# Kernel optimization log

Measured on AMD Instinct MI355X. Metric: run time of the kernel, lower is better.

The kernel has to match this reference:

```python
import jax, jax.numpy as jnp
import numpy as np

B, N, C = 16, 4096, 64
M, K, R = 1024, 32, 0.2
EPS = 1e-5  # BatchNorm eps (eval mode: running_mean=0, running_var=1)


def setup_inputs() -> dict:
    key = jax.random.key(0)
    ks = jax.random.split(key, 8)
    s = 0.05
    return {
        "points": jax.random.normal(ks[0], (B, 3, N), dtype=jnp.float32),
        "features": jax.random.normal(ks[1], (B, C, N), dtype=jnp.float32),
        "w1": jax.random.normal(ks[2], (64, 3 + C), dtype=jnp.float32) * s,
        "b1": jnp.zeros((64,), jnp.float32),
        "g1": jnp.ones((64,), jnp.float32),
        "be1": jnp.zeros((64,), jnp.float32),
        "w2": jax.random.normal(ks[3], (64, 64), dtype=jnp.float32) * s,
        "b2": jnp.zeros((64,), jnp.float32),
        "g2": jnp.ones((64,), jnp.float32),
        "be2": jnp.zeros((64,), jnp.float32),
        "w3": jax.random.normal(ks[4], (128, 64), dtype=jnp.float32) * s,
        "b3": jnp.zeros((128,), jnp.float32),
        "g3": jnp.ones((128,), jnp.float32),
        "be3": jnp.zeros((128,), jnp.float32),
    }


def farthest_point_sampling(pts, m):
    """pts: [B,N,3] -> indices [B,m] (iterative FPS, first point = index 0)."""
    b, n, _ = pts.shape

    def step(carry, _):
        dist, last = carry  # dist [b,n], last [b]
        lastp = jnp.take_along_axis(pts, last[:, None, None], axis=1)  # [b,1,3]
        d = jnp.sum((pts - lastp) ** 2, axis=-1)  # [b,n]
        dist = jnp.minimum(dist, d)
        nxt = jnp.argmax(dist, axis=1).astype(jnp.int32)
        return (dist, nxt), last

    init = (jnp.full((b, n), 1e10, pts.dtype), jnp.zeros((b,), jnp.int32))
    _, idx = jax.lax.scan(step, init, None, length=m)
    return idx.T  # [b,m]


def ball_query(pts, centroids, k, radius):
    """pts [B,N,3], centroids [B,M,3] -> neighbor indices [B,M,K].
    Takes the first k points (by index) within radius; pads with the first hit,
    matching the PointNet++ CUDA ball_query semantics."""
    n = pts.shape[1]
    p2 = jnp.sum(pts ** 2, -1)  # [B,N]
    c2 = jnp.sum(centroids ** 2, -1)  # [B,M]
    d2 = c2[:, :, None] + p2[:, None, :] - 2.0 * jnp.einsum("bmd,bnd->bmn", centroids, pts)
    ar = jnp.arange(n, dtype=jnp.int32)
    key = jnp.where(d2 <= radius * radius, ar[None, None, :], n)  # [B,M,N]
    idx = jnp.sort(key, axis=-1)[..., :k]  # first k in-radius indices (or n)
    first = idx[..., :1]  # centroid itself is always a hit (d2=0)
    idx = jnp.where(idx < n, idx, first)
    return jnp.clip(idx, 0, n - 1)


def _mlp_block(x, w, bias, g, be):
    # 1x1 Conv2d + BatchNorm (eval: mean=0, var=1) + ReLU, x: [B,M,K,Cin]
    y = jnp.einsum("oc,bmkc->bmko", w, x) + bias
    y = y * (g / jnp.sqrt(1.0 + EPS)) + be
    return jax.nn.relu(y)


def reference(points, features, w1, b1, g1, be1, w2, b2, g2, be2, w3, b3, g3, be3):
    pts = jnp.transpose(points, (0, 2, 1))  # [B,N,3]
    feats = jnp.transpose(features, (0, 2, 1))  # [B,N,C]
    b = pts.shape[0]

    cidx = farthest_point_sampling(pts, M)  # [B,M]
    bidx = jnp.arange(b)[:, None]
    cent = pts[bidx, cidx]  # [B,M,3]

    nidx = ball_query(pts, cent, K, R)  # [B,M,K]
    bidx2 = jnp.arange(b)[:, None, None]
    gpts = pts[bidx2, nidx]  # [B,M,K,3]
    gfeat = feats[bidx2, nidx]  # [B,M,K,C]
    local = gpts - cent[:, :, None, :]  # local coords
    x = jnp.concatenate([local, gfeat], axis=-1)  # [B,M,K,3+C]

    x = _mlp_block(x, w1, b1, g1, be1)
    x = _mlp_block(x, w2, b2, g2, be2)
    x = _mlp_block(x, w3, b3, g3, be3)

    out = jnp.max(x, axis=2)  # max over K samples -> [B,M,Cout]
    centroids = jnp.transpose(cent, (0, 2, 1))  # [B,3,M]
    out = jnp.transpose(out, (0, 2, 1))  # [B,Cout,M]
    return centroids, out
```

## Files before the change

kernel.cpp:

```cpp
#include <hip/hip_runtime.h>
#include <math.h>

#define NPTS 4096
#define MC   1024
#define KNB  32

typedef __attribute__((ext_vector_type(8))) short bf16x8;
typedef __attribute__((ext_vector_type(4))) float f32x4;

__device__ __forceinline__ unsigned short f2bf(float f) {
  unsigned int u = __float_as_uint(f);
  u = u + 0x7fffu + ((u >> 16) & 1u);
  return (unsigned short)(u >> 16);
}

template <int CTRL>
__device__ __forceinline__ void dpp_step64(unsigned int& hi, unsigned int& lo) {
  unsigned int ohi = (unsigned int)__builtin_amdgcn_update_dpp((int)hi, (int)hi, CTRL, 0xF, 0xF, false);
  unsigned int olo = (unsigned int)__builtin_amdgcn_update_dpp((int)lo, (int)lo, CTRL, 0xF, 0xF, false);
  if (ohi > hi || (ohi == hi && olo > lo)) { hi = ohi; lo = olo; }
}

__global__ __launch_bounds__(256, 1) void fps_kernel(const float* __restrict__ points,
                                                     float* __restrict__ out_cent) {
  __shared__ float sx[NPTS], sy[NPTS], sz[NPTS];
  __shared__ __align__(16) unsigned long long skey[2][4];
  __shared__ float slog[3][MC];
  const int b = blockIdx.x, t = threadIdx.x;
  const int w = t >> 6, lane = t & 63;
  const float* pb = points + (size_t)b * 3 * NPTS;

  float fx[16], fy[16], fz[16], dist[16];
#pragma unroll
  for (int k = 0; k < 4; ++k) {
    float4 X = ((const float4*)pb)[k * 256 + t];
    float4 Y = ((const float4*)(pb + NPTS))[k * 256 + t];
    float4 Z = ((const float4*)(pb + 2 * NPTS))[k * 256 + t];
    ((float4*)sx)[k * 256 + t] = X;
    ((float4*)sy)[k * 256 + t] = Y;
    ((float4*)sz)[k * 256 + t] = Z;
    fx[k * 4 + 0] = X.x; fx[k * 4 + 1] = X.y; fx[k * 4 + 2] = X.z; fx[k * 4 + 3] = X.w;
    fy[k * 4 + 0] = Y.x; fy[k * 4 + 1] = Y.y; fy[k * 4 + 2] = Y.z; fy[k * 4 + 3] = Y.w;
    fz[k * 4 + 0] = Z.x; fz[k * 4 + 1] = Z.y; fz[k * 4 + 2] = Z.z; fz[k * 4 + 3] = Z.w;
  }
#pragma unroll
  for (int j = 0; j < 16; ++j) dist[j] = 1e10f;
  __syncthreads();

  float lx = sx[0], ly = sy[0], lz = sz[0];

  for (int i = 0; i < MC; ++i) {
    if (t == 0) { slog[0][i] = lx; slog[1][i] = ly; slog[2][i] = lz; }
    if (i == MC - 1) break;

    float bv = -1.0f; int bi = 0;
#pragma unroll
    for (int k = 0; k < 4; ++k)
#pragma unroll
      for (int c = 0; c < 4; ++c) {
        int j = k * 4 + c;
        float dx = __fsub_rn(fx[j], lx);
        float dy = __fsub_rn(fy[j], ly);
        float dz = __fsub_rn(fz[j], lz);
        float d  = __fadd_rn(__fadd_rn(__fmul_rn(dx, dx), __fmul_rn(dy, dy)), __fmul_rn(dz, dz));
        float dm = fminf(dist[j], d);
        dist[j] = dm;
        if (dm > bv) { bv = dm; bi = k * 1024 + t * 4 + c; }
      }

    unsigned int hi = __float_as_uint(bv), lo = ~(unsigned int)bi;
    dpp_step64<0x111>(hi, lo);
    dpp_step64<0x112>(hi, lo);
    dpp_step64<0x114>(hi, lo);
    dpp_step64<0x118>(hi, lo);
    dpp_step64<0x142>(hi, lo);
    dpp_step64<0x143>(hi, lo);

    const int nb = i & 1;
    if (lane == 63) skey[nb][w] = ((unsigned long long)hi << 32) | lo;
    __syncthreads();

    unsigned long long k0 = skey[nb][0], k1 = skey[nb][1];
    unsigned long long k2 = skey[nb][2], k3 = skey[nb][3];
    unsigned long long ka = (k0 > k1) ? k0 : k1;
    unsigned long long kb = (k2 > k3) ? k2 : k3;
    unsigned long long km = (ka > kb) ? ka : kb;
    const int sel = (int)(~(unsigned int)km);

    lx = sx[sel]; ly = sy[sel]; lz = sz[sel];
  }
  __syncthreads();
  float* oc = out_cent + (size_t)b * 3 * MC;
#pragma unroll
  for (int k = 0; k < 12; ++k) {
    int idx = t + k * 256;
    oc[idx] = ((const float*)slog)[idx];
  }
}

__global__ __launch_bounds__(256) void transpose_feats(const float* __restrict__ feats,
                                                       unsigned short* __restrict__ featsT) {
  __shared__ float tile[64][65];
  const int blk = blockIdx.x;
  const int b = blk >> 6;
  const int n0 = (blk & 63) * 64;
  const int t = threadIdx.x;
  const float* src = feats + (size_t)b * 64 * NPTS;
  {
    const int n = t & 63, cbase = t >> 6;
#pragma unroll
    for (int j = 0; j < 16; ++j) {
      int c = cbase + j * 4;
      tile[c][n] = src[(size_t)c * NPTS + n0 + n];
    }
  }
  __syncthreads();
  {
    const int c = t & 63, nbase = t >> 6;
    unsigned short* dst = featsT + ((size_t)b * NPTS + n0) * 64;
#pragma unroll
    for (int j = 0; j < 16; ++j) {
      int n = nbase + j * 4;
      dst[(size_t)n * 64 + c] = f2bf(tile[c][n]);
    }
  }
}

__global__ __launch_bounds__(64) void pack_w(const float* __restrict__ w1,
                                             const float* __restrict__ w2,
                                             const float* __restrict__ w3,
                                             unsigned short* __restrict__ wpack) {
  const int f = blockIdx.x, lane = threadIdx.x;
  int layer, kt, nt;
  if (f < 12)      { layer = 0; kt = f >> 2;        nt = f & 3; }
  else if (f < 20) { layer = 1; kt = (f - 12) >> 2; nt = (f - 12) & 3; }
  else             { layer = 2; kt = (f - 20) >> 3; nt = (f - 20) & 7; }
  const int o = nt * 16 + (lane & 15);
  unsigned short* dst = wpack + ((size_t)f * 64 + lane) * 8;
#pragma unroll
  for (int j = 0; j < 8; ++j) {
    int k = kt * 32 + (lane >> 4) * 8 + j;
    float x = 0.0f;
    if (layer == 0)      { if (k < 67) { int cin = (k < 64) ? (k + 3) : (k - 64); x = w1[o * 67 + cin]; } }
    else if (layer == 1) { x = w2[o * 64 + k]; }
    else                 { x = w3[o * 64 + k]; }
    dst[j] = f2bf(x);
  }
}

__global__ __launch_bounds__(256) void ball_query_kernel(const float* __restrict__ points,
                                                         const float* __restrict__ cent,
                                                         int* __restrict__ nidx) {
  __shared__ float sx[NPTS], sy[NPTS], sz[NPTS];
  __shared__ int lists[4][KNB];
  const int b  = blockIdx.x >> 4;
  const int cb = blockIdx.x & 15;
  const int t = threadIdx.x;
  const float* pb = points + (size_t)b * 3 * NPTS;
#pragma unroll
  for (int j = 0; j < 4; ++j) {
    int i4 = t + j * 256;
    ((float4*)sx)[i4] = ((const float4*)pb)[i4];
    ((float4*)sy)[i4] = ((const float4*)(pb + NPTS))[i4];
    ((float4*)sz)[i4] = ((const float4*)(pb + 2 * NPTS))[i4];
  }
  __syncthreads();
  const int w = t >> 6, lane = t & 63;
  const float R2 = (float)(0.2 * 0.2);
  const float* cbp = cent + (size_t)b * 3 * MC;
  for (int cm = 0; cm < 16; ++cm) {
    const int m  = cb * 64 + w * 16 + cm;
    const int bm = b * MC + m;
    const float cx = cbp[m], cy = cbp[MC + m], cz = cbp[2 * MC + m];
    const float c2 = __fadd_rn(__fadd_rn(__fmul_rn(cx, cx), __fmul_rn(cy, cy)), __fmul_rn(cz, cz));
    int cnt = 0;
    for (int ch = 0; ch < 64; ++ch) {
      const int n = ch * 64 + lane;
      float x = sx[n], y = sy[n], z = sz[n];
      float p2  = __fadd_rn(__fadd_rn(__fmul_rn(x, x),  __fmul_rn(y, y)),  __fmul_rn(z, z));
      float dot = __fadd_rn(__fadd_rn(__fmul_rn(cx, x), __fmul_rn(cy, y)), __fmul_rn(cz, z));
      float d2  = __fsub_rn(__fadd_rn(c2, p2), __fmul_rn(2.0f, dot));
      bool hit = (d2 <= R2);
      unsigned long long msk = __ballot(hit);
      if (hit) {
        int pos = cnt + __popcll(msk & ((1ull << lane) - 1ull));
        if (pos < KNB) lists[w][pos] = n;
      }
      cnt += __popcll(msk);
      if (cnt >= KNB) break;
    }
    if (lane < KNB) {
      int first = lists[w][0];
      int v = (lane < cnt) ? lists[w][lane] : first;
      nidx[(size_t)bm * KNB + lane] = v;
    }
  }
}

__global__ __launch_bounds__(256) void mlp_kernel(
    const float* __restrict__ points,
    const float* __restrict__ cent,
    const int* __restrict__ nidx,
    const unsigned short* __restrict__ featsT,
    const unsigned short* __restrict__ wpack,
    const float* __restrict__ b1, const float* __restrict__ g1, const float* __restrict__ be1,
    const float* __restrict__ b2, const float* __restrict__ g2, const float* __restrict__ be2,
    const float* __restrict__ b3, const float* __restrict__ g3, const float* __restrict__ be3,
    float* __restrict__ out) {
  __shared__ __align__(16) unsigned short Hs[4][2][32 * 72];
  __shared__ __align__(16) float obuf[128 * 20];
  const int t = threadIdx.x;
  const int w = t >> 6, lane = t & 63;
  const int r = lane & 15, q = lane >> 4;
  const float inv_s = 1.0f / sqrtf(1.0f + 1e-5f);

  float pb1[4], ps1[4], pe1[4], pb2[4], ps2[4], pe2[4], pb3[8], ps3[8], pe3[8];
#pragma unroll
  for (int nt = 0; nt < 4; ++nt) {
    int o = nt * 16 + r;
    pb1[nt] = b1[o]; ps1[nt] = g1[o] * inv_s; pe1[nt] = be1[o];
    pb2[nt] = b2[o]; ps2[nt] = g2[o] * inv_s; pe2[nt] = be2[o];
  }
#pragma unroll
  for (int nt = 0; nt < 8; ++nt) {
    int o = nt * 16 + r;
    pb3[nt] = b3[o]; ps3[nt] = g3[o] * inv_s; pe3[nt] = be3[o];
  }
  const int bm0 = blockIdx.x * 16;
  const int b   = bm0 >> 10;
  const int m0  = bm0 & 1023;
  const float* ptsb = points + (size_t)b * 3 * NPTS;
  const float* cbp  = cent + (size_t)b * 3 * MC;

  for (int it = 0; it < 4; ++it) {
    const int ml = it * 4 + w;
    const int bm = bm0 + ml;
    const int m  = bm & 1023;
    const int n0 = nidx[(size_t)bm * KNB + r];
    const int n1 = nidx[(size_t)bm * KNB + 16 + r];
    const float cx = cbp[m], cy = cbp[MC + m], cz = cbp[2 * MC + m];

    bf16x8 aF[2][2];
#pragma unroll
    for (int mt = 0; mt < 2; ++mt) {
      int n = mt ? n1 : n0;
      const unsigned short* rowp = featsT + ((size_t)b * NPTS + n) * 64 + q * 8;
      aF[mt][0] = *(const bf16x8*)(rowp);
      aF[mt][1] = *(const bf16x8*)(rowp + 32);
    }
    bf16x8 aL[2];
#pragma unroll
    for (int mt = 0; mt < 2; ++mt) {
      bf16x8 a = {0, 0, 0, 0, 0, 0, 0, 0};
      if (q == 0) {
        int n = mt ? n1 : n0;
        a[0] = (short)f2bf(ptsb[n] - cx);
        a[1] = (short)f2bf(ptsb[NPTS + n] - cy);
        a[2] = (short)f2bf(ptsb[2 * NPTS + n] - cz);
      }
      aL[mt] = a;
    }
    f32x4 acc1[2][4];
#pragma unroll
    for (int mt = 0; mt < 2; ++mt)
#pragma unroll
      for (int nt = 0; nt < 4; ++nt) acc1[mt][nt] = (f32x4){0.f, 0.f, 0.f, 0.f};
#pragma unroll
    for (int kt = 0; kt < 3; ++kt) {
#pragma unroll
      for (int nt = 0; nt < 4; ++nt) {
        bf16x8 wf = *(const bf16x8*)(wpack + ((size_t)(kt * 4 + nt) * 64 + lane) * 8);
#pragma unroll
        for (int mt = 0; mt < 2; ++mt) {
          bf16x8 a = (kt < 2) ? aF[mt][kt] : aL[mt];
          acc1[mt][nt] = __builtin_amdgcn_mfma_f32_16x16x32_bf16(a, wf, acc1[mt][nt], 0, 0, 0);
        }
      }
    }
#pragma unroll
    for (int mt = 0; mt < 2; ++mt)
#pragma unroll
      for (int nt = 0; nt < 4; ++nt)
#pragma unroll
        for (int rr = 0; rr < 4; ++rr) {
          float y = (acc1[mt][nt][rr] + pb1[nt]) * ps1[nt] + pe1[nt];
          y = fmaxf(y, 0.0f);
          Hs[w][0][(mt * 16 + q * 4 + rr) * 72 + nt * 16 + r] = f2bf(y);
        }
    __threadfence_block();

    f32x4 acc2[2][4];
#pragma unroll
    for (int mt = 0; mt < 2; ++mt)
#pragma unroll
      for (int nt = 0; nt < 4; ++nt) acc2[mt][nt] = (f32x4){0.f, 0.f, 0.f, 0.f};
#pragma unroll
    for (int kt = 0; kt < 2; ++kt) {
      bf16x8 a0 = *(const bf16x8*)&Hs[w][0][(0 * 16 + r) * 72 + kt * 32 + q * 8];
      bf16x8 a1 = *(const bf16x8*)&Hs[w][0][(1 * 16 + r) * 72 + kt * 32 + q * 8];
#pragma unroll
      for (int nt = 0; nt < 4; ++nt) {
        bf16x8 wf = *(const bf16x8*)(wpack + ((size_t)(12 + kt * 4 + nt) * 64 + lane) * 8);
        acc2[0][nt] = __builtin_amdgcn_mfma_f32_16x16x32_bf16(a0, wf, acc2[0][nt], 0, 0, 0);
        acc2[1][nt] = __builtin_amdgcn_mfma_f32_16x16x32_bf16(a1, wf, acc2[1][nt], 0, 0, 0);
      }
    }
#pragma unroll
    for (int mt = 0; mt < 2; ++mt)
#pragma unroll
      for (int nt = 0; nt < 4; ++nt)
#pragma unroll
        for (int rr = 0; rr < 4; ++rr) {
          float y = (acc2[mt][nt][rr] + pb2[nt]) * ps2[nt] + pe2[nt];
          y = fmaxf(y, 0.0f);
          Hs[w][1][(mt * 16 + q * 4 + rr) * 72 + nt * 16 + r] = f2bf(y);
        }
    __threadfence_block();

    f32x4 acc3[2][8];
#pragma unroll
    for (int mt = 0; mt < 2; ++mt)
#pragma unroll
      for (int nt = 0; nt < 8; ++nt) acc3[mt][nt] = (f32x4){0.f, 0.f, 0.f, 0.f};
#pragma unroll
    for (int kt = 0; kt < 2; ++kt) {
      bf16x8 a0 = *(const bf16x8*)&Hs[w][1][(0 * 16 + r) * 72 + kt * 32 + q * 8];
      bf16x8 a1 = *(const bf16x8*)&Hs[w][1][(1 * 16 + r) * 72 + kt * 32 + q * 8];
#pragma unroll
      for (int nt = 0; nt < 8; ++nt) {
        bf16x8 wf = *(const bf16x8*)(wpack + ((size_t)(20 + kt * 8 + nt) * 64 + lane) * 8);
        acc3[0][nt] = __builtin_amdgcn_mfma_f32_16x16x32_bf16(a0, wf, acc3[0][nt], 0, 0, 0);
        acc3[1][nt] = __builtin_amdgcn_mfma_f32_16x16x32_bf16(a1, wf, acc3[1][nt], 0, 0, 0);
      }
    }
#pragma unroll
    for (int nt = 0; nt < 8; ++nt) {
      float pm = 0.0f;
#pragma unroll
      for (int mt = 0; mt < 2; ++mt)
#pragma unroll
        for (int rr = 0; rr < 4; ++rr) {
          float y = (acc3[mt][nt][rr] + pb3[nt]) * ps3[nt] + pe3[nt];
          y = fmaxf(y, 0.0f);
          pm = fmaxf(pm, y);
        }
      pm = fmaxf(pm, __shfl_xor(pm, 16));
      pm = fmaxf(pm, __shfl_xor(pm, 32));
      if (q == 0) obuf[(nt * 16 + r) * 20 + ml] = pm;
    }
    __threadfence_block();
  }
  __syncthreads();
  {
    const int ch = t >> 1, mh = (t & 1) * 8;
    float4 u0 = *(const float4*)&obuf[ch * 20 + mh];
    float4 u1 = *(const float4*)&obuf[ch * 20 + mh + 4];
    float* outp = out + ((size_t)b * 128 + ch) * 1024 + m0 + mh;
    *(float4*)(outp)     = u0;
    *(float4*)(outp + 4) = u1;
  }
}

extern "C" void kernel_launch(void* const* d_in, const int* in_sizes, int n_in,
                              void* d_out, int out_size, void* d_ws, size_t ws_size,
                              hipStream_t stream) {
  (void)in_sizes; (void)n_in; (void)out_size; (void)ws_size;
  const float* points   = (const float*)d_in[0];
  const float* features = (const float*)d_in[1];
  const float* w1  = (const float*)d_in[2];
  const float* b1  = (const float*)d_in[3];
  const float* g1  = (const float*)d_in[4];
  const float* be1 = (const float*)d_in[5];
  const float* w2  = (const float*)d_in[6];
  const float* b2  = (const float*)d_in[7];
  const float* g2  = (const float*)d_in[8];
  const float* be2 = (const float*)d_in[9];
  const float* w3  = (const float*)d_in[10];
  const float* b3  = (const float*)d_in[11];
  const float* g3  = (const float*)d_in[12];
  const float* be3 = (const float*)d_in[13];

  float* outc = (float*)d_out;
  float* outf = outc + 16 * 3 * 1024;

  char* ws = (char*)d_ws;
  int*            nidx    = (int*)(ws);
  unsigned short* featsT  = (unsigned short*)(ws + 0x200000);
  unsigned short* wpack   = (unsigned short*)(ws + 0xA00000);

  fps_kernel<<<16, 256, 0, stream>>>(points, outc);
  transpose_feats<<<1024, 256, 0, stream>>>(features, featsT);
  pack_w<<<36, 64, 0, stream>>>(w1, w2, w3, wpack);
  ball_query_kernel<<<256, 256, 0, stream>>>(points, outc, nidx);
  mlp_kernel<<<1024, 256, 0, stream>>>(points, outc, nidx, featsT, wpack,
                                       b1, g1, be1, b2, g2, be2, b3, g3, be3, outf);
}
```

Measured before the change: 1.106 ms.

## Fuse FPS, feature transpose and weight packing into one launch; ballot-based argmax

Merges the three preprocessing kernels into one launch, dispatching on block index, so the transpose and weight packing run alongside the long serial FPS blocks instead of after them. The FPS inner loop now keeps only a float max, reduces it with DPP, and recovers the lowest matching index with ballots, instead of carrying a 64-bit value/index key through every DPP step. This shortens the per-iteration critical path of the serial FPS loop. The cost is extra ballot and scalar work per iteration, and the FPS blocks now share one launch with the transpose and pack blocks and use a shared-memory union.

Result: faster. 979.7 us (-11.5%).

```diff
diff --git a/kernel.cpp b/kernel.cpp
--- a/kernel.cpp
+++ b/kernel.cpp
@@ -15,136 +15,164 @@
 }
 
 template <int CTRL>
-__device__ __forceinline__ void dpp_step64(unsigned int& hi, unsigned int& lo) {
-  unsigned int ohi = (unsigned int)__builtin_amdgcn_update_dpp((int)hi, (int)hi, CTRL, 0xF, 0xF, false);
-  unsigned int olo = (unsigned int)__builtin_amdgcn_update_dpp((int)lo, (int)lo, CTRL, 0xF, 0xF, false);
-  if (ohi > hi || (ohi == hi && olo > lo)) { hi = ohi; lo = olo; }
-}
-
-__global__ __launch_bounds__(256, 1) void fps_kernel(const float* __restrict__ points,
-                                                     float* __restrict__ out_cent) {
-  __shared__ float sx[NPTS], sy[NPTS], sz[NPTS];
-  __shared__ __align__(16) unsigned long long skey[2][4];
-  __shared__ float slog[3][MC];
-  const int b = blockIdx.x, t = threadIdx.x;
-  const int w = t >> 6, lane = t & 63;
-  const float* pb = points + (size_t)b * 3 * NPTS;
-
-  float fx[16], fy[16], fz[16], dist[16];
-#pragma unroll
-  for (int k = 0; k < 4; ++k) {
-    float4 X = ((const float4*)pb)[k * 256 + t];
-    float4 Y = ((const float4*)(pb + NPTS))[k * 256 + t];
-    float4 Z = ((const float4*)(pb + 2 * NPTS))[k * 256 + t];
-    ((float4*)sx)[k * 256 + t] = X;
-    ((float4*)sy)[k * 256 + t] = Y;
-    ((float4*)sz)[k * 256 + t] = Z;
-    fx[k * 4 + 0] = X.x; fx[k * 4 + 1] = X.y; fx[k * 4 + 2] = X.z; fx[k * 4 + 3] = X.w;
-    fy[k * 4 + 0] = Y.x; fy[k * 4 + 1] = Y.y; fy[k * 4 + 2] = Y.z; fy[k * 4 + 3] = Y.w;
-    fz[k * 4 + 0] = Z.x; fz[k * 4 + 1] = Z.y; fz[k * 4 + 2] = Z.z; fz[k * 4 + 3] = Z.w;
-  }
-#pragma unroll
-  for (int j = 0; j < 16; ++j) dist[j] = 1e10f;
-  __syncthreads();
-
-  float lx = sx[0], ly = sy[0], lz = sz[0];
-
-  for (int i = 0; i < MC; ++i) {
-    if (t == 0) { slog[0][i] = lx; slog[1][i] = ly; slog[2][i] = lz; }
-    if (i == MC - 1) break;
-
-    float bv = -1.0f; int bi = 0;
-#pragma unroll
-    for (int k = 0; k < 4; ++k)
-#pragma unroll
-      for (int c = 0; c < 4; ++c) {
-        int j = k * 4 + c;
+__device__ __forceinline__ float dpp_max(float v) {
+  int o = __builtin_amdgcn_update_dpp(__float_as_int(v), __float_as_int(v), CTRL, 0xF, 0xF, false);
+  return fmaxf(v, __int_as_float(o));
+}
+
+struct FpsShared {
+  float sx[NPTS], sy[NPTS], sz[NPTS];
+  unsigned long long skey[2][4];
+  float slog[3][MC];
+};
+struct TransShared {
+  float tile[64][65];
+};
+
+__global__ __launch_bounds__(256, 1) void fused_pre(
+    const float* __restrict__ points, const float* __restrict__ feats,
+    const float* __restrict__ w1, const float* __restrict__ w2,
+    const float* __restrict__ w3,
+    unsigned short* __restrict__ featsT, unsigned short* __restrict__ wpack,
+    float* __restrict__ out_cent) {
+  __shared__ union { FpsShared f; TransShared tr; } S;
+  const int blk = blockIdx.x;
+  const int t = threadIdx.x;
+
+  if (blk < 16) {
+    const int b = blk;
+    const int w = t >> 6;
+    const float* pb = points + (size_t)b * 3 * NPTS;
+
+    float fx[16], fy[16], fz[16], dist[16];
+#pragma unroll
+    for (int k = 0; k < 4; ++k) {
+      float4 X = ((const float4*)pb)[k * 256 + t];
+      float4 Y = ((const float4*)(pb + NPTS))[k * 256 + t];
+      float4 Z = ((const float4*)(pb + 2 * NPTS))[k * 256 + t];
+      ((float4*)S.f.sx)[k * 256 + t] = X;
+      ((float4*)S.f.sy)[k * 256 + t] = Y;
+      ((float4*)S.f.sz)[k * 256 + t] = Z;
+      fx[k * 4 + 0] = X.x; fx[k * 4 + 1] = X.y; fx[k * 4 + 2] = X.z; fx[k * 4 + 3] = X.w;
+      fy[k * 4 + 0] = Y.x; fy[k * 4 + 1] = Y.y; fy[k * 4 + 2] = Y.z; fy[k * 4 + 3] = Y.w;
+      fz[k * 4 + 0] = Z.x; fz[k * 4 + 1] = Z.y; fz[k * 4 + 2] = Z.z; fz[k * 4 + 3] = Z.w;
+    }
+#pragma unroll
+    for (int j = 0; j < 16; ++j) dist[j] = 1e10f;
+    __syncthreads();
+
+    float lx = S.f.sx[0], ly = S.f.sy[0], lz = S.f.sz[0];
+
+    for (int i = 0; i < MC; ++i) {
+      if (t == 0) { S.f.slog[0][i] = lx; S.f.slog[1][i] = ly; S.f.slog[2][i] = lz; }
+      if (i == MC - 1) break;
+
+      float m = -1.0f;
+#pragma unroll
+      for (int j = 0; j < 16; ++j) {
         float dx = __fsub_rn(fx[j], lx);
         float dy = __fsub_rn(fy[j], ly);
         float dz = __fsub_rn(fz[j], lz);
         float d  = __fadd_rn(__fadd_rn(__fmul_rn(dx, dx), __fmul_rn(dy, dy)), __fmul_rn(dz, dz));
         float dm = fminf(dist[j], d);
         dist[j] = dm;
-        if (dm > bv) { bv = dm; bi = k * 1024 + t * 4 + c; }
-      }
-
-    unsigned int hi = __float_as_uint(bv), lo = ~(unsigned int)bi;
-    dpp_step64<0x111>(hi, lo);
-    dpp_step64<0x112>(hi, lo);
-    dpp_step64<0x114>(hi, lo);
-    dpp_step64<0x118>(hi, lo);
-    dpp_step64<0x142>(hi, lo);
-    dpp_step64<0x143>(hi, lo);
-
-    const int nb = i & 1;
-    if (lane == 63) skey[nb][w] = ((unsigned long long)hi << 32) | lo;
+        m = fmaxf(m, dm);
+      }
+
+      m = dpp_max<0x111>(m);
+      m = dpp_max<0x112>(m);
+      m = dpp_max<0x114>(m);
+      m = dpp_max<0x118>(m);
+      m = dpp_max<0x142>(m);
+      m = dpp_max<0x143>(m);
+      const float wv = __int_as_float(__builtin_amdgcn_readlane(__float_as_int(m), 63));
+
+      unsigned long long mk[4][4];
+#pragma unroll
+      for (int k = 0; k < 4; ++k) {
+        mk[k][0] = __ballot(dist[k * 4 + 0] == wv);
+        mk[k][1] = __ballot(dist[k * 4 + 1] == wv);
+        mk[k][2] = __ballot(dist[k * 4 + 2] == wv);
+        mk[k][3] = __ballot(dist[k * 4 + 3] == wv);
+      }
+      unsigned long long s0 = 0, s1 = 0, s2 = 0, s3 = 0, anyk = 0;
+      int sk = -1;
+#pragma unroll
+      for (int k = 0; k < 4; ++k) {
+        unsigned long long a = mk[k][0] | mk[k][1] | mk[k][2] | mk[k][3];
+        if (sk < 0 && a != 0ull) {
+          sk = k; anyk = a;
+          s0 = mk[k][0]; s1 = mk[k][1]; s2 = mk[k][2]; s3 = mk[k][3];
+        }
+      }
+      const int l = __builtin_ctzll(anyk);
+      const unsigned long long bit = 1ull << l;
+      const int c = (s0 & bit) ? 0 : (s1 & bit) ? 1 : (s2 & bit) ? 2 : 3;
+      const int selIdx = sk * 1024 + 256 * w + 4 * l + c;
+
+      const int nb = i & 1;
+      if ((t & 63) == 0)
+        S.f.skey[nb][w] = ((unsigned long long)__float_as_uint(wv) << 32) | (unsigned int)~selIdx;
+      __syncthreads();
+
+      unsigned long long k0 = S.f.skey[nb][0], k1 = S.f.skey[nb][1];
+      unsigned long long k2 = S.f.skey[nb][2], k3 = S.f.skey[nb][3];
+      unsigned long long ka = (k0 > k1) ? k0 : k1;
+      unsigned long long kb = (k2 > k3) ? k2 : k3;
+      unsigned long long km = (ka > kb) ? ka : kb;
+      const int sel = (int)(~(unsigned int)km);
+      lx = S.f.sx[sel]; ly = S.f.sy[sel]; lz = S.f.sz[sel];
+    }
     __syncthreads();
-
-    unsigned long long k0 = skey[nb][0], k1 = skey[nb][1];
-    unsigned long long k2 = skey[nb][2], k3 = skey[nb][3];
-    unsigned long long ka = (k0 > k1) ? k0 : k1;
-    unsigned long long kb = (k2 > k3) ? k2 : k3;
-    unsigned long long km = (ka > kb) ? ka : kb;
-    const int sel = (int)(~(unsigned int)km);
-
-    lx = sx[sel]; ly = sy[sel]; lz = sz[sel];
-  }
-  __syncthreads();
-  float* oc = out_cent + (size_t)b * 3 * MC;
-#pragma unroll
-  for (int k = 0; k < 12; ++k) {
-    int idx = t + k * 256;
-    oc[idx] = ((const float*)slog)[idx];
-  }
-}
-
-__global__ __launch_bounds__(256) void transpose_feats(const float* __restrict__ feats,
-                                                       unsigned short* __restrict__ featsT) {
-  __shared__ float tile[64][65];
-  const int blk = blockIdx.x;
-  const int b = blk >> 6;
-  const int n0 = (blk & 63) * 64;
-  const int t = threadIdx.x;
-  const float* src = feats + (size_t)b * 64 * NPTS;
-  {
-    const int n = t & 63, cbase = t >> 6;
-#pragma unroll
-    for (int j = 0; j < 16; ++j) {
-      int c = cbase + j * 4;
-      tile[c][n] = src[(size_t)c * NPTS + n0 + n];
-    }
-  }
-  __syncthreads();
-  {
-    const int c = t & 63, nbase = t >> 6;
-    unsigned short* dst = featsT + ((size_t)b * NPTS + n0) * 64;
-#pragma unroll
-    for (int j = 0; j < 16; ++j) {
-      int n = nbase + j * 4;
-      dst[(size_t)n * 64 + c] = f2bf(tile[c][n]);
-    }
-  }
-}
-
-__global__ __launch_bounds__(64) void pack_w(const float* __restrict__ w1,
-                                             const float* __restrict__ w2,
-                                             const float* __restrict__ w3,
-                                             unsigned short* __restrict__ wpack) {
-  const int f = blockIdx.x, lane = threadIdx.x;
-  int layer, kt, nt;
-  if (f < 12)      { layer = 0; kt = f >> 2;        nt = f & 3; }
-  else if (f < 20) { layer = 1; kt = (f - 12) >> 2; nt = (f - 12) & 3; }
-  else             { layer = 2; kt = (f - 20) >> 3; nt = (f - 20) & 7; }
-  const int o = nt * 16 + (lane & 15);
-  unsigned short* dst = wpack + ((size_t)f * 64 + lane) * 8;
-#pragma unroll
-  for (int j = 0; j < 8; ++j) {
-    int k = kt * 32 + (lane >> 4) * 8 + j;
-    float x = 0.0f;
-    if (layer == 0)      { if (k < 67) { int cin = (k < 64) ? (k + 3) : (k - 64); x = w1[o * 67 + cin]; } }
-    else if (layer == 1) { x = w2[o * 64 + k]; }
-    else                 { x = w3[o * 64 + k]; }
-    dst[j] = f2bf(x);
+    float* oc = out_cent + (size_t)b * 3 * MC;
+#pragma unroll
+    for (int k = 0; k < 12; ++k) {
+      int idx = t + k * 256;
+      oc[idx] = ((const float*)S.f.slog)[idx];
+    }
+  } else if (blk < 16 + 1024) {
+    const int rel = blk - 16;
+    const int b = rel >> 6;
+    const int n0 = (rel & 63) * 64;
+    const float* src = feats + (size_t)b * 64 * NPTS;
+    {
+      const int n = t & 63, cbase = t >> 6;
+#pragma unroll
+      for (int j = 0; j < 16; ++j) {
+        int cc = cbase + j * 4;
+        S.tr.tile[cc][n] = src[(size_t)cc * NPTS + n0 + n];
+      }
+    }
+    __syncthreads();
+    {
+      const int cc = t & 63, nbase = t >> 6;
+      unsigned short* dst = featsT + ((size_t)b * NPTS + n0) * 64;
+#pragma unroll
+      for (int j = 0; j < 16; ++j) {
+        int n = nbase + j * 4;
+        dst[(size_t)n * 64 + cc] = f2bf(S.tr.tile[cc][n]);
+      }
+    }
+  } else {
+    const int f = (blk - (16 + 1024)) * 4 + (t >> 6);
+    const int lane = t & 63;
+    if (f < 36) {
+      int layer, kt, nt;
+      if (f < 12)      { layer = 0; kt = f >> 2;        nt = f & 3; }
+      else if (f < 20) { layer = 1; kt = (f - 12) >> 2; nt = (f - 12) & 3; }
+      else             { layer = 2; kt = (f - 20) >> 3; nt = (f - 20) & 7; }
+      const int o = nt * 16 + (lane & 15);
+      unsigned short* dst = wpack + ((size_t)f * 64 + lane) * 8;
+#pragma unroll
+      for (int j = 0; j < 8; ++j) {
+        int k = kt * 32 + (lane >> 4) * 8 + j;
+        float x = 0.0f;
+        if (layer == 0)      { if (k < 67) { int cin = (k < 64) ? (k + 3) : (k - 64); x = w1[o * 67 + cin]; } }
+        else if (layer == 1) { x = w2[o * 64 + k]; }
+        else                 { x = w3[o * 64 + k]; }
+        dst[j] = f2bf(x);
+      }
+    }
   }
 }
 
@@ -388,9 +416,8 @@
   unsigned short* featsT  = (unsigned short*)(ws + 0x200000);
   unsigned short* wpack   = (unsigned short*)(ws + 0xA00000);
 
-  fps_kernel<<<16, 256, 0, stream>>>(points, outc);
-  transpose_feats<<<1024, 256, 0, stream>>>(features, featsT);
-  pack_w<<<36, 64, 0, stream>>>(w1, w2, w3, wpack);
+  fused_pre<<<16 + 1024 + 9, 256, 0, stream>>>(points, features, w1, w2, w3,
+                                               featsT, wpack, outc);
   ball_query_kernel<<<256, 256, 0, stream>>>(points, outc, nidx);
   mlp_kernel<<<1024, 256, 0, stream>>>(points, outc, nidx, featsT, wpack,
                                        b1, g1, be1, b2, g2, be2, b3, g3, be3, outf);
```
